# Kernel optimization log

Measured on AMD Instinct MI355X. Metric: run time of the kernel, lower is better.

## Reference

```python
import jax, jax.numpy as jnp
import numpy as np

T, N, D = 8, 4096, 1024
MARGIN, WEIGHT, LOWE_RATIO = 1.1, 1.0, 0.9


def _normalize(x, eps=1e-12):
    # F.normalize(x, dim=-1)
    return x / jnp.maximum(jnp.linalg.norm(x, axis=-1, keepdims=True), eps)


def _cdist(a, b):
    # Euclidean distance matrix [Na, Nb]
    d2 = (jnp.sum(a * a, axis=1)[:, None]
          + jnp.sum(b * b, axis=1)[None, :]
          - 2.0 * a @ b.T)
    return jnp.sqrt(jnp.maximum(d2, 0.0))


def setup_inputs() -> dict:
    key = jax.random.key(0)
    k1, k2 = jax.random.split(key)
    superfeatures = jax.random.normal(k1, (T, N, D), dtype=jnp.float32)
    attention = jax.random.uniform(k2, (T, N), dtype=jnp.float32)
    return {"superfeatures": superfeatures, "attention": attention}


def reference(superfeatures, attention):
    q = _normalize(superfeatures[0])          # [N, D] query feats
    p = _normalize(superfeatures[1])          # [N, D] positive feats
    negs = _normalize(superfeatures[2:])      # [nneg, N, D]

    # ---- match_attn: mutual NN + Lowe ratio + attention top-half mask ----
    dist = _cdist(q, p)                       # [N, N]
    best1 = jnp.argmin(dist, axis=1)          # per-query nearest pos
    best2 = jnp.argmin(dist, axis=0)          # per-pos nearest query
    ar = jnp.arange(N)
    reciprocal = best1[best2] == ar
    dist2 = dist.at[best2, ar].set(jnp.inf)   # knock out best per column
    second_min = jnp.min(dist2, axis=0)       # second-best per column
    ratio1to2 = dist[best2, ar] / second_min
    _, top_idx = jax.lax.top_k(attention[1], N // 2)
    att_mask = jnp.zeros((N,), dtype=jnp.float32).at[top_idx].set(1.0)
    valid = reciprocal & (ratio1to2 <= LOWE_RATIO) & (att_mask > 0)

    # anchors per positive index j: query[best2[j]] (masked rows zeroed later)
    anchors = q[best2]                        # [N, D]
    dpos = jnp.sum((anchors - p) ** 2, axis=1)  # [N]

    # hard-negative mining per negative image (indices are non-differentiable)
    def per_neg(nf):
        d = _cdist(jax.lax.stop_gradient(anchors), jax.lax.stop_gradient(nf))
        nidx = jnp.argmin(d, axis=1)
        nsel = nf[nidx]                       # [N, D]
        return jnp.sum((anchors - nsel) ** 2, axis=1)

    dnegs = jax.vmap(per_neg)(negs)           # [nneg, N]

    hinge = jnp.maximum(dpos[None, :] - dnegs + MARGIN, 0.0)
    loss = jnp.sum(hinge * valid[None, :].astype(hinge.dtype))
    return loss * WEIGHT
```

## Files before the change

kernel.cpp:

```cpp
#include <hip/hip_runtime.h>
#include <cstdint>
#include <cstddef>

#define NTOT 4096
#define DIM  1024
#define NNEG 6
#define KTOP 2048

using u32 = unsigned int;
using u64 = unsigned long long;

typedef __attribute__((ext_vector_type(8))) short bf16x8;
typedef __attribute__((ext_vector_type(4))) float f32x4;

__device__ __forceinline__ u32 monoU(float f){
  u32 b = __float_as_uint(f);
  return (b & 0x80000000u) ? ~b : (b | 0x80000000u);
}

__device__ __forceinline__ short f2bf(float f){
  u32 x = __float_as_uint(f);
  u32 r = x + 0x7FFFu + ((x >> 16) & 1u);
  return (short)(r >> 16);
}

__device__ __forceinline__ void gload16(const short* g, short* l){
  __builtin_amdgcn_global_load_lds(
      (const __attribute__((address_space(1))) void*)(g),
      (__attribute__((address_space(3))) void*)(l), 16, 0, 0);
}

__device__ __forceinline__ float blockSumAll(float v){
  __shared__ float lds[4];
  for (int o = 32; o; o >>= 1) v += __shfl_down(v, o);
  if ((threadIdx.x & 63) == 0) lds[threadIdx.x >> 6] = v;
  __syncthreads();
  float r = lds[0] + lds[1] + lds[2] + lds[3];
  __syncthreads();
  return r;
}

__global__ void initK(u64* __restrict__ nidxp, u64* __restrict__ best1p,
                      double* __restrict__ lossAcc){
  int i = blockIdx.x * 256 + threadIdx.x;
  if (i < NNEG * NTOT) nidxp[i] = ~0ULL;
  if (i < NTOT) best1p[i] = ~0ULL;
  if (i == 0) *lossAcc = 0.0;
}

__global__ __launch_bounds__(256) void rowNormPackK(const float* __restrict__ sf,
    float* __restrict__ norms, float* __restrict__ sumn, short* __restrict__ packbf){
  int row = blockIdx.x;
  const float* x = sf + (size_t)row * DIM;
  float4 v = reinterpret_cast<const float4*>(x)[threadIdx.x];
  float s = blockSumAll(v.x*v.x + v.y*v.y + v.z*v.z + v.w*v.w);
  float t = fmaxf(sqrtf(s), 1e-12f);
  float inv = 1.0f / t;
  float a0 = v.x*inv, a1 = v.y*inv, a2 = v.z*inv, a3 = v.w*inv;
  float s2 = blockSumAll(a0*a0 + a1*a1 + a2*a2 + a3*a3);
  short4 pk; pk.x = f2bf(a0); pk.y = f2bf(a1); pk.z = f2bf(a2); pk.w = f2bf(a3);
  reinterpret_cast<short4*>(packbf + (size_t)row * DIM)[threadIdx.x] = pk;
  if (threadIdx.x == 0){ norms[row] = t; sumn[row] = s2; }
}

__global__ __launch_bounds__(1024) void topkMaskK(const float* __restrict__ att,
                                                  float* __restrict__ mask){
  __shared__ u32 hist[256];
  __shared__ u32 sprefix, sremain;
  __shared__ u32 scan[1024];
  int tid = threadIdx.x;
  u32 u[4];
  #pragma unroll
  for (int e = 0; e < 4; ++e) u[e] = monoU(att[tid*4 + e]);
  if (tid == 0){ sprefix = 0u; sremain = KTOP; }
  __syncthreads();
  for (int shift = 24; shift >= 0; shift -= 8){
    if (tid < 256) hist[tid] = 0u;
    __syncthreads();
    u32 pfx = sprefix;
    #pragma unroll
    for (int e = 0; e < 4; ++e){
      bool cand = (shift == 24) || ((u[e] >> (shift + 8)) == (pfx >> (shift + 8)));
      if (cand) atomicAdd(&hist[(u[e] >> shift) & 255u], 1u);
    }
    __syncthreads();
    if (tid == 0){
      u32 rem = sremain, cum = 0; int b = 255;
      for (; b >= 0; --b){ cum += hist[b]; if (cum >= rem) break; }
      sprefix = pfx | ((u32)b << shift);
      sremain = rem - (cum - hist[b]);
    }
    __syncthreads();
  }
  u32 T = sprefix, need = sremain;
  u32 c = 0;
  #pragma unroll
  for (int e = 0; e < 4; ++e) c += (u[e] == T);
  scan[tid] = c; __syncthreads();
  for (int d = 1; d < 1024; d <<= 1){
    u32 add = (tid >= d) ? scan[tid - d] : 0u;
    __syncthreads();
    scan[tid] += add;
    __syncthreads();
  }
  u32 excl = scan[tid] - c;
  #pragma unroll
  for (int e = 0; e < 4; ++e){
    bool m;
    if (u[e] > T) m = true;
    else if (u[e] == T){ m = (excl < need); excl++; }
    else m = false;
    mask[tid*4 + e] = m ? 1.0f : 0.0f;
  }
}

template<bool GATHER>
__global__ __launch_bounds__(256) void distMfmaK(
    const short* __restrict__ packbf, const float* __restrict__ sumn,
    const int* __restrict__ best2, u64* __restrict__ rowMinP,
    float* __restrict__ cm1, int* __restrict__ cr1, float* __restrict__ cm2)
{
  __shared__ __align__(16) short As[128*32];
  __shared__ __align__(16) short Bs[128*32];
  const int bi = blockIdx.y, bj = blockIdx.x;
  const int fB = GATHER ? (2 + blockIdx.z) : 1;
  const short* Abf = packbf;
  const short* Bbf = packbf + (size_t)fB * NTOT * DIM;
  const float* sumB = sumn + fB * NTOT;
  u64* rmp = GATHER ? (rowMinP + (size_t)blockIdx.z * NTOT) : rowMinP;

  const int tid  = threadIdx.x;
  const int lane = tid & 63, wv = tid >> 6;
  const int wr = wv >> 1, wc = wv & 1;

  const int rs0 = wv*32 + (lane>>2);
  const int rs1 = rs0 + 16;
  const int sl  = lane & 3;
  const int ka0 = (sl ^ ((rs0 >> 1) & 3)) << 3;
  const int ka1 = (sl ^ ((rs1 >> 1) & 3)) << 3;
  const int ga0 = bi*128 + rs0, ga1 = bi*128 + rs1;
  const int ar0 = GATHER ? best2[ga0] : ga0;
  const int ar1 = GATHER ? best2[ga1] : ga1;
  const short* aS0 = Abf + (size_t)ar0 * DIM + ka0;
  const short* aS1 = Abf + (size_t)ar1 * DIM + ka1;
  const short* bS0 = Bbf + (size_t)(bj*128 + rs0) * DIM + ka0;
  const short* bS1 = Bbf + (size_t)(bj*128 + rs1) * DIM + ka1;
  short* aD0 = As + (wv*32)*32;
  short* aD1 = As + (wv*32 + 16)*32;
  short* bD0 = Bs + (wv*32)*32;
  short* bD1 = Bs + (wv*32 + 16)*32;

  const int fra  = wr*64 + (lane & 15);
  const int frb  = wc*64 + (lane & 15);
  const int kblk = lane >> 4;
  const int aoff = fra*32 + ((kblk ^ ((fra >> 1) & 3)) << 3);
  const int boff = frb*32 + ((kblk ^ ((frb >> 1) & 3)) << 3);

  f32x4 acc[4][4] = {};

  for (int k0 = 0; k0 < DIM; k0 += 32){
    gload16(aS0 + k0, aD0);
    gload16(aS1 + k0, aD1);
    gload16(bS0 + k0, bD0);
    gload16(bS1 + k0, bD1);
    __syncthreads();
    bf16x8 af[4], bfr[4];
    #pragma unroll
    for (int m = 0; m < 4; ++m) af[m]  = *(const bf16x8*)(As + aoff + m*512);
    #pragma unroll
    for (int n = 0; n < 4; ++n) bfr[n] = *(const bf16x8*)(Bs + boff + n*512);
    #pragma unroll
    for (int m = 0; m < 4; ++m)
      #pragma unroll
      for (int n = 0; n < 4; ++n)
        acc[m][n] = __builtin_amdgcn_mfma_f32_16x16x32_bf16(af[m], bfr[n], acc[m][n], 0, 0, 0);
    __syncthreads();
  }

  const int q = lane >> 4;
  float sb[4];
  #pragma unroll
  for (int n = 0; n < 4; ++n) sb[n] = sumB[bj*128 + wc*64 + n*16 + (lane & 15)];
  #pragma unroll
  for (int m = 0; m < 4; ++m){
    #pragma unroll
    for (int r = 0; r < 4; ++r){
      u64 mk = ~0ULL;
      #pragma unroll
      for (int n = 0; n < 4; ++n){
        float key = sb[n] - 2.0f * acc[m][n][r];
        int gj = bj*128 + wc*64 + n*16 + (lane & 15);
        u64 pk = ((u64)monoU(key) << 32) | (u32)gj;
        if (pk < mk) mk = pk;
      }
      #pragma unroll
      for (int off = 1; off <= 8; off <<= 1){
        u64 o = __shfl_xor((unsigned long long)mk, off);
        if (o < mk) mk = o;
      }
      if ((lane & 15) == 0)
        atomicMin(&rmp[bi*128 + wr*64 + m*16 + q*4 + r], mk);
    }
  }

  if constexpr (!GATHER){
    float* Lm1 = reinterpret_cast<float*>(As);
    int*   Lr1 = reinterpret_cast<int*>(As) + 1024;
    float* Lm2 = reinterpret_cast<float*>(Bs);
    const float* sumA = sumn;
    const int gibase = bi*128 + wr*64;
    #pragma unroll
    for (int n = 0; n < 4; ++n){
      float m1 = INFINITY, m2 = INFINITY; int r1 = 0;
      #pragma unroll
      for (int m = 0; m < 4; ++m)
        #pragma unroll
        for (int r = 0; r < 4; ++r){
          int gi = gibase + m*16 + q*4 + r;
          float v = sumA[gi] - 2.0f * acc[m][n][r];
          if (v < m1){ m2 = m1; m1 = v; r1 = gi; }
          else m2 = fminf(m2, v);
        }
      int c = wc*64 + n*16 + (lane & 15);
      int contrib = wr*4 + q;
      Lm1[c*8 + contrib] = m1;
      Lr1[c*8 + contrib] = r1;
      Lm2[c*8 + contrib] = m2;
    }
    __syncthreads();
    if (tid < 128){
      float M1 = Lm1[tid*8], M2 = Lm2[tid*8]; int R1 = Lr1[tid*8];
      #pragma unroll
      for (int c2 = 1; c2 < 8; ++c2){
        float v1 = Lm1[tid*8 + c2], v2 = Lm2[tid*8 + c2]; int rr = Lr1[tid*8 + c2];
        if (v1 < M1 || (v1 == M1 && rr < R1)){
          M2 = fminf(M2, M1); M1 = v1; R1 = rr; M2 = fminf(M2, v2);
        } else M2 = fminf(M2, v1);
      }
      int gc = bj*128 + tid;
      cm1[(size_t)bi*NTOT + gc] = M1;
      cr1[(size_t)bi*NTOT + gc] = R1;
      cm2[(size_t)bi*NTOT + gc] = M2;
    }
  }
}

__global__ __launch_bounds__(256) void colMergeK(const float* __restrict__ cm1,
    const int* __restrict__ cr1, const float* __restrict__ cm2,
    const float* __restrict__ sumnP, int* __restrict__ best2, int* __restrict__ ratioOk){
  int j = blockIdx.x * 256 + threadIdx.x;
  float M1 = cm1[j]; int R1 = cr1[j]; float M2 = cm2[j];
  for (int c = 1; c < 32; ++c){
    size_t o = (size_t)c * NTOT + j;
    float v1 = cm1[o]; int rr = cr1[o]; float v2 = cm2[o];
    if (v1 < M1 || (v1 == M1 && rr < R1)){
      M2 = fminf(M2, M1); M1 = v1; R1 = rr; M2 = fminf(M2, v2);
    } else M2 = fminf(M2, v1);
  }
  best2[j] = R1;
  float sbj = sumnP[j];
  float d1 = sqrtf(fmaxf(M1 + sbj, 0.0f));
  float ds = sqrtf(fmaxf(M2 + sbj, 0.0f));
  ratioOk[j] = (d1 / ds <= 0.9f) ? 1 : 0;
}

__global__ __launch_bounds__(256) void validDposK(const float* __restrict__ sf,
    const float* __restrict__ norms, const u64* __restrict__ best1p,
    const int* __restrict__ best2, const int* __restrict__ ratioOk,
    const float* __restrict__ attm, float* __restrict__ valid, float* __restrict__ dpos){
  int j = blockIdx.x;
  int b2 = best2[j];
  const float* qr = sf + (size_t)b2 * DIM;
  const float* pr = sf + (size_t)(NTOT + j) * DIM;
  float tq = norms[b2], tp = norms[NTOT + j];
  float4 qv = reinterpret_cast<const float4*>(qr)[threadIdx.x];
  float4 pv = reinterpret_cast<const float4*>(pr)[threadIdx.x];
  float d0 = qv.x/tq - pv.x/tp, d1 = qv.y/tq - pv.y/tp;
  float d2 = qv.z/tq - pv.z/tp, d3 = qv.w/tq - pv.w/tp;
  float s = blockSumAll(d0*d0 + d1*d1 + d2*d2 + d3*d3);
  if (threadIdx.x == 0){
    dpos[j] = s;
    int b1 = (int)(best1p[b2] & 0xFFFFFFFFu);
    bool ok = (b1 == j) && (ratioOk[j] != 0) && (attm[j] > 0.0f);
    valid[j] = ok ? 1.0f : 0.0f;
  }
}

__global__ __launch_bounds__(256) void dnegHingeK(const float* __restrict__ sf,
    const float* __restrict__ norms, const int* __restrict__ best2,
    const u64* __restrict__ nidxp, const float* __restrict__ valid,
    const float* __restrict__ dpos, double* __restrict__ lossAcc){
  int j = blockIdx.x, t = blockIdx.y;
  int nidx = (int)(nidxp[(size_t)t * NTOT + j] & 0xFFFFFFFFu);
  int b2 = best2[j];
  const float* ar = sf + (size_t)b2 * DIM;
  const float* nr = sf + (size_t)((2 + t) * NTOT + nidx) * DIM;
  float ta = norms[b2], tn = norms[(2 + t) * NTOT + nidx];
  float4 av = reinterpret_cast<const float4*>(ar)[threadIdx.x];
  float4 nv = reinterpret_cast<const float4*>(nr)[threadIdx.x];
  float d0 = av.x/ta - nv.x/tn, d1 = av.y/ta - nv.y/tn;
  float d2 = av.z/ta - nv.z/tn, d3 = av.w/ta - nv.w/tn;
  float s = blockSumAll(d0*d0 + d1*d1 + d2*d2 + d3*d3);
  if (threadIdx.x == 0 && valid[j] > 0.0f){
    float h = fmaxf(dpos[j] - s + 1.1f, 0.0f);
    if (h > 0.0f) atomicAdd(lossAcc, (double)h);
  }
}

__global__ void finK(const double* __restrict__ lossAcc, float* __restrict__ out){
  out[0] = (float)(*lossAcc);
}

extern "C" void kernel_launch(void* const* d_in, const int* in_sizes, int n_in,
                              void* d_out, int out_size, void* d_ws, size_t ws_size,
                              hipStream_t stream){
  const float* sf  = (const float*)d_in[0];
  const float* att = (const float*)d_in[1];
  char* w = (char*)d_ws;
  size_t off = 0;
  auto alloc = [&](size_t bytes)->void*{
    off = (off + 255) & ~(size_t)255;
    void* p = w + off; off += bytes; return p;
  };
  short* packbf = (short*)alloc((size_t)8 * NTOT * DIM * 2);
  float* norms  = (float*)alloc((size_t)8 * NTOT * 4);
  float* sumn   = (float*)alloc((size_t)8 * NTOT * 4);
  float* attm   = (float*)alloc((size_t)NTOT * 4);
  u64*   best1p = (u64*)  alloc((size_t)NTOT * 8);
  int*   best2  = (int*)  alloc((size_t)NTOT * 4);
  int*   ratOk  = (int*)  alloc((size_t)NTOT * 4);
  float* valid  = (float*)alloc((size_t)NTOT * 4);
  float* dpos   = (float*)alloc((size_t)NTOT * 4);
  u64*   nidxp  = (u64*)  alloc((size_t)NNEG * NTOT * 8);
  float* cm1    = (float*)alloc((size_t)32 * NTOT * 4);
  int*   cr1    = (int*)  alloc((size_t)32 * NTOT * 4);
  float* cm2    = (float*)alloc((size_t)32 * NTOT * 4);
  double* lossAcc = (double*)alloc(8);

  initK<<<dim3((NNEG*NTOT + 255)/256), dim3(256), 0, stream>>>(nidxp, best1p, lossAcc);
  rowNormPackK<<<dim3(8*NTOT), dim3(256), 0, stream>>>(sf, norms, sumn, packbf);
  topkMaskK<<<dim3(1), dim3(1024), 0, stream>>>(att + NTOT, attm);
  distMfmaK<false><<<dim3(32,32,1), dim3(256), 0, stream>>>(
      packbf, sumn, nullptr, best1p, cm1, cr1, cm2);
  colMergeK<<<dim3(16), dim3(256), 0, stream>>>(cm1, cr1, cm2, sumn + NTOT, best2, ratOk);
  validDposK<<<dim3(NTOT), dim3(256), 0, stream>>>(sf, norms, best1p, best2, ratOk, attm, valid, dpos);
  distMfmaK<true><<<dim3(32,32,NNEG), dim3(256), 0, stream>>>(
      packbf, sumn, best2, nidxp, nullptr, nullptr, nullptr);
  dnegHingeK<<<dim3(NTOT, NNEG), dim3(256), 0, stream>>>(sf, norms, best2, nidxp, valid, dpos, lossAcc);
  finK<<<dim3(1), dim3(1), 0, stream>>>(lossAcc, (float*)d_out);
}
```

Baseline: 587.4 us.

## Use 32x32 MFMA with BK=64 tiles, warp-level row norms, fuse tail kernels

The distance GEMM switches from 16x16x32 to 32x32x16 bf16 MFMA with a 64-wide K step and a new LDS swizzle. This halves the number of K iterations and barriers, and the column-min epilogue now merges across wave halves with shuffles. Row normalisation uses one wave per row instead of block reductions. The top-k scans use wave shuffles, and the dpos/valid and hinge kernels are fused into one kernel that skips invalid rows early. The larger tiles and accumulators raise register use.

```diff
diff --git a/kernel.cpp b/kernel.cpp
--- a/kernel.cpp
+++ b/kernel.cpp
@@ -6,12 +6,13 @@
 #define DIM  1024
 #define NNEG 6
 #define KTOP 2048
+#define BK   64
 
 using u32 = unsigned int;
 using u64 = unsigned long long;
 
 typedef __attribute__((ext_vector_type(8))) short bf16x8;
-typedef __attribute__((ext_vector_type(4))) float f32x4;
+typedef __attribute__((ext_vector_type(16))) float f32x16;
 
 __device__ __forceinline__ u32 monoU(float f){
   u32 b = __float_as_uint(f);
@@ -50,60 +51,98 @@
 
 __global__ __launch_bounds__(256) void rowNormPackK(const float* __restrict__ sf,
     float* __restrict__ norms, float* __restrict__ sumn, short* __restrict__ packbf){
-  int row = blockIdx.x;
-  const float* x = sf + (size_t)row * DIM;
-  float4 v = reinterpret_cast<const float4*>(x)[threadIdx.x];
-  float s = blockSumAll(v.x*v.x + v.y*v.y + v.z*v.z + v.w*v.w);
+  const int wv = threadIdx.x >> 6, lane = threadIdx.x & 63;
+  const int row = blockIdx.x * 4 + wv;
+  const float4* x = reinterpret_cast<const float4*>(sf + (size_t)row * DIM);
+  float4 v[4];
+  float s = 0.0f;
+  #pragma unroll
+  for (int i = 0; i < 4; ++i){
+    v[i] = x[lane + 64*i];
+    s += v[i].x*v[i].x + v[i].y*v[i].y + v[i].z*v[i].z + v[i].w*v[i].w;
+  }
+  #pragma unroll
+  for (int o = 1; o <= 32; o <<= 1) s += __shfl_xor(s, o);
   float t = fmaxf(sqrtf(s), 1e-12f);
   float inv = 1.0f / t;
-  float a0 = v.x*inv, a1 = v.y*inv, a2 = v.z*inv, a3 = v.w*inv;
-  float s2 = blockSumAll(a0*a0 + a1*a1 + a2*a2 + a3*a3);
-  short4 pk; pk.x = f2bf(a0); pk.y = f2bf(a1); pk.z = f2bf(a2); pk.w = f2bf(a3);
-  reinterpret_cast<short4*>(packbf + (size_t)row * DIM)[threadIdx.x] = pk;
-  if (threadIdx.x == 0){ norms[row] = t; sumn[row] = s2; }
+  float s2 = 0.0f;
+  short4* pb = reinterpret_cast<short4*>(packbf + (size_t)row * DIM);
+  #pragma unroll
+  for (int i = 0; i < 4; ++i){
+    float a0 = v[i].x*inv, a1 = v[i].y*inv, a2 = v[i].z*inv, a3 = v[i].w*inv;
+    s2 += a0*a0 + a1*a1 + a2*a2 + a3*a3;
+    short4 pk; pk.x = f2bf(a0); pk.y = f2bf(a1); pk.z = f2bf(a2); pk.w = f2bf(a3);
+    pb[lane + 64*i] = pk;
+  }
+  #pragma unroll
+  for (int o = 1; o <= 32; o <<= 1) s2 += __shfl_xor(s2, o);
+  if (lane == 0){ norms[row] = t; sumn[row] = s2; }
 }
 
 __global__ __launch_bounds__(1024) void topkMaskK(const float* __restrict__ att,
                                                   float* __restrict__ mask){
   __shared__ u32 hist[256];
+  __shared__ u32 Csuf[257];
+  __shared__ u32 wsum[16];
   __shared__ u32 sprefix, sremain;
-  __shared__ u32 scan[1024];
-  int tid = threadIdx.x;
+  const int tid = threadIdx.x, lane = tid & 63, wv = tid >> 6;
   u32 u[4];
   #pragma unroll
   for (int e = 0; e < 4; ++e) u[e] = monoU(att[tid*4 + e]);
   if (tid == 0){ sprefix = 0u; sremain = KTOP; }
-  __syncthreads();
   for (int shift = 24; shift >= 0; shift -= 8){
+    __syncthreads();
+    u32 pfx = sprefix, rem = sremain;
     if (tid < 256) hist[tid] = 0u;
     __syncthreads();
-    u32 pfx = sprefix;
     #pragma unroll
     for (int e = 0; e < 4; ++e){
       bool cand = (shift == 24) || ((u[e] >> (shift + 8)) == (pfx >> (shift + 8)));
       if (cand) atomicAdd(&hist[(u[e] >> shift) & 255u], 1u);
     }
     __syncthreads();
-    if (tid == 0){
-      u32 rem = sremain, cum = 0; int b = 255;
-      for (; b >= 0; --b){ cum += hist[b]; if (cum >= rem) break; }
-      sprefix = pfx | ((u32)b << shift);
-      sremain = rem - (cum - hist[b]);
-    }
-    __syncthreads();
-  }
+    u32 p = 0;
+    if (tid < 256){
+      p = hist[255 - tid];
+      #pragma unroll
+      for (int o = 1; o <= 32; o <<= 1){
+        u32 t = __shfl_up(p, o);
+        if (lane >= o) p += t;
+      }
+      if (lane == 63) wsum[wv] = p;
+    }
+    __syncthreads();
+    if (tid < 256){
+      u32 base = 0;
+      for (int w = 0; w < wv; ++w) base += wsum[w];
+      Csuf[255 - tid] = base + p;
+      if (tid == 0) Csuf[256] = 0u;
+    }
+    __syncthreads();
+    if (tid < 256){
+      u32 Cb = Csuf[tid], Cb1 = Csuf[tid + 1];
+      if (Cb >= rem && Cb1 < rem){
+        sprefix = pfx | ((u32)tid << shift);
+        sremain = rem - Cb1;
+      }
+    }
+  }
+  __syncthreads();
   u32 T = sprefix, need = sremain;
   u32 c = 0;
   #pragma unroll
   for (int e = 0; e < 4; ++e) c += (u[e] == T);
-  scan[tid] = c; __syncthreads();
-  for (int d = 1; d < 1024; d <<= 1){
-    u32 add = (tid >= d) ? scan[tid - d] : 0u;
-    __syncthreads();
-    scan[tid] += add;
-    __syncthreads();
-  }
-  u32 excl = scan[tid] - c;
+  u32 p = c;
+  #pragma unroll
+  for (int o = 1; o <= 32; o <<= 1){
+    u32 t = __shfl_up(p, o);
+    if (lane >= o) p += t;
+  }
+  if (lane == 63) wsum[wv] = p;
+  __syncthreads();
+  u32 base = 0;
+  for (int w = 0; w < wv; ++w) base += wsum[w];
+  u32 excl = base + p - c;
   #pragma unroll
   for (int e = 0; e < 4; ++e){
     bool m;
@@ -120,8 +159,8 @@
     const int* __restrict__ best2, u64* __restrict__ rowMinP,
     float* __restrict__ cm1, int* __restrict__ cr1, float* __restrict__ cm2)
 {
-  __shared__ __align__(16) short As[128*32];
-  __shared__ __align__(16) short Bs[128*32];
+  __shared__ __align__(16) short As[128*BK];
+  __shared__ __align__(16) short Bs[128*BK];
   const int bi = blockIdx.y, bj = blockIdx.x;
   const int fB = GATHER ? (2 + blockIdx.z) : 1;
   const short* Abf = packbf;
@@ -129,118 +168,131 @@
   const float* sumB = sumn + fB * NTOT;
   u64* rmp = GATHER ? (rowMinP + (size_t)blockIdx.z * NTOT) : rowMinP;
 
-  const int tid  = threadIdx.x;
+  const int tid = threadIdx.x;
   const int lane = tid & 63, wv = tid >> 6;
   const int wr = wv >> 1, wc = wv & 1;
 
-  const int rs0 = wv*32 + (lane>>2);
-  const int rs1 = rs0 + 16;
-  const int sl  = lane & 3;
-  const int ka0 = (sl ^ ((rs0 >> 1) & 3)) << 3;
-  const int ka1 = (sl ^ ((rs1 >> 1) & 3)) << 3;
-  const int ga0 = bi*128 + rs0, ga1 = bi*128 + rs1;
-  const int ar0 = GATHER ? best2[ga0] : ga0;
-  const int ar1 = GATHER ? best2[ga1] : ga1;
-  const short* aS0 = Abf + (size_t)ar0 * DIM + ka0;
-  const short* aS1 = Abf + (size_t)ar1 * DIM + ka1;
-  const short* bS0 = Bbf + (size_t)(bj*128 + rs0) * DIM + ka0;
-  const short* bS1 = Bbf + (size_t)(bj*128 + rs1) * DIM + ka1;
-  short* aD0 = As + (wv*32)*32;
-  short* aD1 = As + (wv*32 + 16)*32;
-  short* bD0 = Bs + (wv*32)*32;
-  short* bD1 = Bs + (wv*32 + 16)*32;
-
-  const int fra  = wr*64 + (lane & 15);
-  const int frb  = wc*64 + (lane & 15);
-  const int kblk = lane >> 4;
-  const int aoff = fra*32 + ((kblk ^ ((fra >> 1) & 3)) << 3);
-  const int boff = frb*32 + ((kblk ^ ((frb >> 1) & 3)) << 3);
-
-  f32x4 acc[4][4] = {};
-
-  for (int k0 = 0; k0 < DIM; k0 += 32){
-    gload16(aS0 + k0, aD0);
-    gload16(aS1 + k0, aD1);
-    gload16(bS0 + k0, bD0);
-    gload16(bS1 + k0, bD1);
-    __syncthreads();
-    bf16x8 af[4], bfr[4];
-    #pragma unroll
-    for (int m = 0; m < 4; ++m) af[m]  = *(const bf16x8*)(As + aoff + m*512);
-    #pragma unroll
-    for (int n = 0; n < 4; ++n) bfr[n] = *(const bf16x8*)(Bs + boff + n*512);
-    #pragma unroll
-    for (int m = 0; m < 4; ++m)
-      #pragma unroll
-      for (int n = 0; n < 4; ++n)
-        acc[m][n] = __builtin_amdgcn_mfma_f32_16x16x32_bf16(af[m], bfr[n], acc[m][n], 0, 0, 0);
-    __syncthreads();
-  }
-
-  const int q = lane >> 4;
-  float sb[4];
-  #pragma unroll
-  for (int n = 0; n < 4; ++n) sb[n] = sumB[bj*128 + wc*64 + n*16 + (lane & 15)];
-  #pragma unroll
-  for (int m = 0; m < 4; ++m){
-    #pragma unroll
-    for (int r = 0; r < 4; ++r){
-      u64 mk = ~0ULL;
-      #pragma unroll
-      for (int n = 0; n < 4; ++n){
-        float key = sb[n] - 2.0f * acc[m][n][r];
-        int gj = bj*128 + wc*64 + n*16 + (lane & 15);
-        u64 pk = ((u64)monoU(key) << 32) | (u32)gj;
-        if (pk < mk) mk = pk;
-      }
-      #pragma unroll
-      for (int off = 1; off <= 8; off <<= 1){
-        u64 o = __shfl_xor((unsigned long long)mk, off);
-        if (o < mk) mk = o;
-      }
-      if ((lane & 15) == 0)
-        atomicMin(&rmp[bi*128 + wr*64 + m*16 + q*4 + r], mk);
+  const short* aS[4]; const short* bS[4]; short* aD[4]; short* bD[4];
+  #pragma unroll
+  for (int s = 0; s < 4; ++s){
+    const int r = wv*32 + s*8 + (lane >> 3);
+    const int chunk = (lane & 7) ^ (lane >> 3);
+    const int garow = bi*128 + r;
+    const int arow = GATHER ? best2[garow] : garow;
+    aS[s] = Abf + (size_t)arow * DIM + chunk*8;
+    bS[s] = Bbf + (size_t)(bj*128 + r) * DIM + chunk*8;
+    aD[s] = As + (wv*32 + s*8) * BK;
+    bD[s] = Bs + (wv*32 + s*8) * BK;
+  }
+
+  const int lane31 = lane & 31, kh = lane >> 5, l7 = lane & 7;
+  int offA[2][4], offB[2][4];
+  #pragma unroll
+  for (int m = 0; m < 2; ++m)
+    #pragma unroll
+    for (int ks = 0; ks < 4; ++ks){
+      const int sl = ((ks*2 + kh) ^ l7) << 3;
+      offA[m][ks] = (wr*64 + m*32 + lane31)*BK + sl;
+      offB[m][ks] = (wc*64 + m*32 + lane31)*BK + sl;
+    }
+
+  f32x16 acc[2][2] = {};
+
+  for (int k0 = 0; k0 < DIM; k0 += BK){
+    #pragma unroll
+    for (int s = 0; s < 4; ++s) gload16(aS[s] + k0, aD[s]);
+    #pragma unroll
+    for (int s = 0; s < 4; ++s) gload16(bS[s] + k0, bD[s]);
+    __syncthreads();
+    bf16x8 af[2][4], bfv[2][4];
+    #pragma unroll
+    for (int m = 0; m < 2; ++m)
+      #pragma unroll
+      for (int ks = 0; ks < 4; ++ks){
+        af[m][ks]  = *(const bf16x8*)(As + offA[m][ks]);
+        bfv[m][ks] = *(const bf16x8*)(Bs + offB[m][ks]);
+      }
+    #pragma unroll
+    for (int ks = 0; ks < 4; ++ks)
+      #pragma unroll
+      for (int m = 0; m < 2; ++m)
+        #pragma unroll
+        for (int n = 0; n < 2; ++n)
+          acc[m][n] = __builtin_amdgcn_mfma_f32_32x32x16_bf16(
+              af[m][ks], bfv[n][ks], acc[m][n], 0, 0, 0);
+    __syncthreads();
+  }
+
+  const int c0 = bj*128 + wc*64 + lane31;
+  const float sb0 = sumB[c0];
+  const float sb1 = sumB[c0 + 32];
+  #pragma unroll
+  for (int m = 0; m < 2; ++m){
+    #pragma unroll
+    for (int reg = 0; reg < 16; ++reg){
+      const int rloc = (reg & 3) + 8*(reg >> 2) + 4*kh;
+      const int grow = bi*128 + wr*64 + m*32 + rloc;
+      float k0v = sb0 - 2.0f * acc[m][0][reg];
+      float k1v = sb1 - 2.0f * acc[m][1][reg];
+      u64 pk  = ((u64)monoU(k0v) << 32) | (u32)c0;
+      u64 pk1 = ((u64)monoU(k1v) << 32) | (u32)(c0 + 32);
+      if (pk1 < pk) pk = pk1;
+      #pragma unroll
+      for (int off = 1; off <= 16; off <<= 1){
+        u64 o = __shfl_xor(pk, off);
+        if (o < pk) pk = o;
+      }
+      if (lane31 == 0) atomicMin(&rmp[grow], pk);
     }
   }
 
   if constexpr (!GATHER){
-    float* Lm1 = reinterpret_cast<float*>(As);
-    int*   Lr1 = reinterpret_cast<int*>(As) + 1024;
-    float* Lm2 = reinterpret_cast<float*>(Bs);
-    const float* sumA = sumn;
     const int gibase = bi*128 + wr*64;
-    #pragma unroll
-    for (int n = 0; n < 4; ++n){
+    float M1[2], M2[2]; int R1[2];
+    #pragma unroll
+    for (int n = 0; n < 2; ++n){
       float m1 = INFINITY, m2 = INFINITY; int r1 = 0;
       #pragma unroll
-      for (int m = 0; m < 4; ++m)
+      for (int m = 0; m < 2; ++m)
         #pragma unroll
-        for (int r = 0; r < 4; ++r){
-          int gi = gibase + m*16 + q*4 + r;
-          float v = sumA[gi] - 2.0f * acc[m][n][r];
-          if (v < m1){ m2 = m1; m1 = v; r1 = gi; }
+        for (int reg = 0; reg < 16; ++reg){
+          const int rloc = (reg & 3) + 8*(reg >> 2) + 4*kh;
+          const int grow = gibase + m*32 + rloc;
+          float v = sumn[grow] - 2.0f * acc[m][n][reg];
+          if (v < m1){ m2 = m1; m1 = v; r1 = grow; }
           else m2 = fminf(m2, v);
         }
-      int c = wc*64 + n*16 + (lane & 15);
-      int contrib = wr*4 + q;
-      Lm1[c*8 + contrib] = m1;
-      Lr1[c*8 + contrib] = r1;
-      Lm2[c*8 + contrib] = m2;
+      float o1 = __shfl_xor(m1, 32), o2 = __shfl_xor(m2, 32);
+      int   oR = __shfl_xor(r1, 32);
+      if (o1 < m1 || (o1 == m1 && oR < r1)){
+        m2 = fminf(m2, m1); m1 = o1; r1 = oR; m2 = fminf(m2, o2);
+      } else m2 = fminf(m2, o1);
+      M1[n] = m1; M2[n] = m2; R1[n] = r1;
+    }
+    __syncthreads();
+    float* Lm1 = reinterpret_cast<float*>(As);
+    int*   Lr1 = reinterpret_cast<int*>(As) + 256;
+    float* Lm2 = reinterpret_cast<float*>(As) + 512;
+    if (kh == 0){
+      #pragma unroll
+      for (int n = 0; n < 2; ++n){
+        const int c = wc*64 + n*32 + lane31;
+        Lm1[c*2 + wr] = M1[n];
+        Lr1[c*2 + wr] = R1[n];
+        Lm2[c*2 + wr] = M2[n];
+      }
     }
     __syncthreads();
     if (tid < 128){
-      float M1 = Lm1[tid*8], M2 = Lm2[tid*8]; int R1 = Lr1[tid*8];
-      #pragma unroll
-      for (int c2 = 1; c2 < 8; ++c2){
-        float v1 = Lm1[tid*8 + c2], v2 = Lm2[tid*8 + c2]; int rr = Lr1[tid*8 + c2];
-        if (v1 < M1 || (v1 == M1 && rr < R1)){
-          M2 = fminf(M2, M1); M1 = v1; R1 = rr; M2 = fminf(M2, v2);
-        } else M2 = fminf(M2, v1);
-      }
-      int gc = bj*128 + tid;
-      cm1[(size_t)bi*NTOT + gc] = M1;
-      cr1[(size_t)bi*NTOT + gc] = R1;
-      cm2[(size_t)bi*NTOT + gc] = M2;
+      float A1 = Lm1[tid*2],   A2 = Lm2[tid*2];   int Ar = Lr1[tid*2];
+      float B1 = Lm1[tid*2+1], B2 = Lm2[tid*2+1]; int Br = Lr1[tid*2+1];
+      float M1f, M2f; int R1f;
+      if (B1 < A1 || (B1 == A1 && Br < Ar)){ M1f = B1; R1f = Br; M2f = fminf(B2, A1); }
+      else                                 { M1f = A1; R1f = Ar; M2f = fminf(A2, B1); }
+      const int gc = bj*128 + tid;
+      cm1[(size_t)bi*NTOT + gc] = M1f;
+      cr1[(size_t)bi*NTOT + gc] = R1f;
+      cm2[(size_t)bi*NTOT + gc] = M2f;
     }
   }
 }
@@ -264,47 +316,33 @@
   ratioOk[j] = (d1 / ds <= 0.9f) ? 1 : 0;
 }
 
-__global__ __launch_bounds__(256) void validDposK(const float* __restrict__ sf,
+__global__ __launch_bounds__(256) void tailK(const float* __restrict__ sf,
     const float* __restrict__ norms, const u64* __restrict__ best1p,
     const int* __restrict__ best2, const int* __restrict__ ratioOk,
-    const float* __restrict__ attm, float* __restrict__ valid, float* __restrict__ dpos){
-  int j = blockIdx.x;
-  int b2 = best2[j];
-  const float* qr = sf + (size_t)b2 * DIM;
-  const float* pr = sf + (size_t)(NTOT + j) * DIM;
-  float tq = norms[b2], tp = norms[NTOT + j];
-  float4 qv = reinterpret_cast<const float4*>(qr)[threadIdx.x];
-  float4 pv = reinterpret_cast<const float4*>(pr)[threadIdx.x];
-  float d0 = qv.x/tq - pv.x/tp, d1 = qv.y/tq - pv.y/tp;
-  float d2 = qv.z/tq - pv.z/tp, d3 = qv.w/tq - pv.w/tp;
-  float s = blockSumAll(d0*d0 + d1*d1 + d2*d2 + d3*d3);
-  if (threadIdx.x == 0){
-    dpos[j] = s;
-    int b1 = (int)(best1p[b2] & 0xFFFFFFFFu);
-    bool ok = (b1 == j) && (ratioOk[j] != 0) && (attm[j] > 0.0f);
-    valid[j] = ok ? 1.0f : 0.0f;
-  }
-}
-
-__global__ __launch_bounds__(256) void dnegHingeK(const float* __restrict__ sf,
-    const float* __restrict__ norms, const int* __restrict__ best2,
-    const u64* __restrict__ nidxp, const float* __restrict__ valid,
-    const float* __restrict__ dpos, double* __restrict__ lossAcc){
-  int j = blockIdx.x, t = blockIdx.y;
-  int nidx = (int)(nidxp[(size_t)t * NTOT + j] & 0xFFFFFFFFu);
-  int b2 = best2[j];
-  const float* ar = sf + (size_t)b2 * DIM;
-  const float* nr = sf + (size_t)((2 + t) * NTOT + nidx) * DIM;
-  float ta = norms[b2], tn = norms[(2 + t) * NTOT + nidx];
-  float4 av = reinterpret_cast<const float4*>(ar)[threadIdx.x];
-  float4 nv = reinterpret_cast<const float4*>(nr)[threadIdx.x];
-  float d0 = av.x/ta - nv.x/tn, d1 = av.y/ta - nv.y/tn;
-  float d2 = av.z/ta - nv.z/tn, d3 = av.w/ta - nv.w/tn;
-  float s = blockSumAll(d0*d0 + d1*d1 + d2*d2 + d3*d3);
-  if (threadIdx.x == 0 && valid[j] > 0.0f){
-    float h = fmaxf(dpos[j] - s + 1.1f, 0.0f);
-    if (h > 0.0f) atomicAdd(lossAcc, (double)h);
-  }
+    const float* __restrict__ attm, const u64* __restrict__ nidxp,
+    double* __restrict__ lossAcc){
+  const int j = blockIdx.x;
+  const int b2 = best2[j];
+  bool ok = ((int)(best1p[b2] & 0xFFFFFFFFu) == j) && (ratioOk[j] != 0) && (attm[j] > 0.0f);
+  if (!ok) return;
+  const float ta = norms[b2];
+  float4 av = reinterpret_cast<const float4*>(sf + (size_t)b2 * DIM)[threadIdx.x];
+  const float a0 = av.x/ta, a1 = av.y/ta, a2 = av.z/ta, a3 = av.w/ta;
+  const float tp = norms[NTOT + j];
+  float4 pv = reinterpret_cast<const float4*>(sf + (size_t)(NTOT + j) * DIM)[threadIdx.x];
+  float d0 = a0 - pv.x/tp, d1 = a1 - pv.y/tp, d2 = a2 - pv.z/tp, d3 = a3 - pv.w/tp;
+  float dpos = blockSumAll(d0*d0 + d1*d1 + d2*d2 + d3*d3);
+  float lsum = 0.0f;
+  for (int t = 0; t < NNEG; ++t){
+    int nidx = (int)(nidxp[(size_t)t * NTOT + j] & 0xFFFFFFFFu);
+    int nrow = (2 + t) * NTOT + nidx;
+    float tn = norms[nrow];
+    float4 nv = reinterpret_cast<const float4*>(sf + (size_t)nrow * DIM)[threadIdx.x];
+    float e0 = a0 - nv.x/tn, e1 = a1 - nv.y/tn, e2 = a2 - nv.z/tn, e3 = a3 - nv.w/tn;
+    float dn = blockSumAll(e0*e0 + e1*e1 + e2*e2 + e3*e3);
+    lsum += fmaxf(dpos - dn + 1.1f, 0.0f);
+  }
+  if (threadIdx.x == 0 && lsum > 0.0f) atomicAdd(lossAcc, (double)lsum);
 }
 
 __global__ void finK(const double* __restrict__ lossAcc, float* __restrict__ out){
@@ -329,23 +367,20 @@
   u64*   best1p = (u64*)  alloc((size_t)NTOT * 8);
   int*   best2  = (int*)  alloc((size_t)NTOT * 4);
   int*   ratOk  = (int*)  alloc((size_t)NTOT * 4);
-  float* valid  = (float*)alloc((size_t)NTOT * 4);
-  float* dpos   = (float*)alloc((size_t)NTOT * 4);
   u64*   nidxp  = (u64*)  alloc((size_t)NNEG * NTOT * 8);
   float* cm1    = (float*)alloc((size_t)32 * NTOT * 4);
   int*   cr1    = (int*)  alloc((size_t)32 * NTOT * 4);
   float* cm2    = (float*)alloc((size_t)32 * NTOT * 4);
   double* lossAcc = (double*)alloc(8);
 
-  initK<<<dim3((NNEG*NTOT + 255)/256), dim3(256), 0, stream>>>(nidxp, best1p, lossAcc);
-  rowNormPackK<<<dim3(8*NTOT), dim3(256), 0, stream>>>(sf, norms, sumn, packbf);
+  initK<<<dim3(96), dim3(256), 0, stream>>>(nidxp, best1p, lossAcc);
+  rowNormPackK<<<dim3(8192), dim3(256), 0, stream>>>(sf, norms, sumn, packbf);
   topkMaskK<<<dim3(1), dim3(1024), 0, stream>>>(att + NTOT, attm);
   distMfmaK<false><<<dim3(32,32,1), dim3(256), 0, stream>>>(
       packbf, sumn, nullptr, best1p, cm1, cr1, cm2);
   colMergeK<<<dim3(16), dim3(256), 0, stream>>>(cm1, cr1, cm2, sumn + NTOT, best2, ratOk);
-  validDposK<<<dim3(NTOT), dim3(256), 0, stream>>>(sf, norms, best1p, best2, ratOk, attm, valid, dpos);
   distMfmaK<true><<<dim3(32,32,NNEG), dim3(256), 0, stream>>>(
       packbf, sumn, best2, nidxp, nullptr, nullptr, nullptr);
-  dnegHingeK<<<dim3(NTOT, NNEG), dim3(256), 0, stream>>>(sf, norms, best2, nidxp, valid, dpos, lossAcc);
+  tailK<<<dim3(NTOT), dim3(256), 0, stream>>>(sf, norms, best1p, best2, ratOk, attm, nidxp, lossAcc);
   finK<<<dim3(1), dim3(1), 0, stream>>>(lossAcc, (float*)d_out);
 }
```

Result: no change. 597.8 us (+1.8%).
